# Kernel optimization log

Measured on AMD Instinct MI355X. Metric: run time of the kernel, lower is better.

Reference implementation:

```python
import jax, jax.numpy as jnp
import numpy as np

B, T, D, H = 8, 4096, 512, 512


def setup_inputs() -> dict:
    key = jax.random.key(0)
    k1, k2, k3, k4, k5, k6 = jax.random.split(key, 6)
    lim = 1.0 / np.sqrt(D)
    return {
        "x": jax.random.normal(k1, (B, T, D), dtype=jnp.float32),
        "h_0": jax.random.normal(k2, (B, 1, H), dtype=jnp.float32),
        "W_z": jax.random.uniform(k3, (H, D), jnp.float32, -lim, lim),
        "b_z": jax.random.uniform(k4, (H,), jnp.float32, -lim, lim),
        "W_h": jax.random.uniform(k5, (H, D), jnp.float32, -lim, lim),
        "b_h": jax.random.uniform(k6, (H,), jnp.float32, -lim, lim),
    }


def reference(x, h_0, W_z, b_z, W_h, b_h):
    # z_t = sigmoid(W_z x_t), h~_t = tanh(W_h x_t)
    z = jax.nn.sigmoid(jnp.einsum('btd,hd->bth', x, W_z) + b_z)  # (B,T,H)
    h_tilde = jnp.tanh(jnp.einsum('btd,hd->bth', x, W_h) + b_h)  # (B,T,H)
    a = 1.0 - z            # multiplicative coeffs
    b = z * h_tilde        # additive terms (b[:,0] handled as h0 carry)

    # linear recurrence h_t = a_t * h_{t-1} + b_t, h_0 given
    def scan_fn(h_prev, ab):
        a_t, b_t = ab
        h_t = a_t * h_prev + b_t
        return h_t, h_t

    a_t = jnp.swapaxes(a, 0, 1)  # (T,B,H)
    b_t = jnp.swapaxes(b, 0, 1)  # (T,B,H)
    _, hs = jax.lax.scan(scan_fn, h_0[:, 0, :], (a_t, b_t))
    return jnp.swapaxes(hs, 0, 1)  # (B,T,H)
```

## Files before the change

kernel.cpp:

```cpp
#include <hip/hip_runtime.h>

constexpr int Bn = 8, Tn = 4096, Dn = 512, Hn = 512;
constexpr int Mn = Bn * Tn;
constexpr int BM = 128, BHt = 128, BK = 32;
constexpr int NKT = Dn / BK;
constexpr int CH = 64, NC = Tn / CH;

typedef __attribute__((ext_vector_type(8))) short s8v;
typedef __attribute__((ext_vector_type(4))) float f4v;
typedef __attribute__((ext_vector_type(8))) _Float16 h8v;
typedef unsigned short ushort_t;

typedef __attribute__((address_space(1))) const void gv_t;
typedef __attribute__((address_space(3))) void lv_t;

__device__ __forceinline__ short f2bf(float f) {
  unsigned u = __float_as_uint(f);
  u = (u + 0x7fffu + ((u >> 16) & 1u)) >> 16;
  return (short)u;
}

__global__ __launch_bounds__(256) void convert_all(
    const float* __restrict__ X, const float* __restrict__ Wz,
    const float* __restrict__ Wh, ushort_t* __restrict__ Xb,
    ushort_t* __restrict__ Wzb, ushort_t* __restrict__ Whb) {
  int bx = blockIdx.x, tid = threadIdx.x;
  const float* src;
  ushort_t* dst;
  int lb;
  if (bx < 4096)      { src = X;  dst = Xb;  lb = bx; }
  else if (bx < 4160) { src = Wz; dst = Wzb; lb = bx - 4096; }
  else                { src = Wh; dst = Whb; lb = bx - 4160; }
  const float* tsrc = src + ((size_t)(lb >> 4) * 128) * Dn + (lb & 15) * BK;
#pragma unroll
  for (int p = 0; p < 2; p++) {
    int idx = tid + p * 256;
    int r = idx >> 2, k8 = idx & 3;
    const float4* sv = reinterpret_cast<const float4*>(tsrc + (size_t)r * Dn + k8 * 8);
    float4 f0 = sv[0], f1 = sv[1];
    s8v v;
    v[0] = f2bf(f0.x); v[1] = f2bf(f0.y); v[2] = f2bf(f0.z); v[3] = f2bf(f0.w);
    v[4] = f2bf(f1.x); v[5] = f2bf(f1.y); v[6] = f2bf(f1.z); v[7] = f2bf(f1.w);
    int c = (r >> 4) * 64 + k8 * 16 + (r & 15);
    *reinterpret_cast<s8v*>(&dst[((size_t)lb * 512 + c) * 8]) = v;
  }
}

__global__ __launch_bounds__(256) void gemm_act(
    const ushort_t* __restrict__ Xb, const ushort_t* __restrict__ Wzb,
    const ushort_t* __restrict__ Whb,
    const float* __restrict__ bzp, const float* __restrict__ bhp,
    h8v* __restrict__ cab) {
  __shared__ __align__(16) ushort_t lds[2][3 * 4096];

  int tid = threadIdx.x, lane = tid & 63, wid = tid >> 6;
  int wr = wid >> 1, wc = wid & 1;
  int bm = blockIdx.x, bhb = blockIdx.y;

  const ushort_t* xs = Xb + (size_t)bm * NKT * 4096;
  const ushort_t* zs = Wzb + (size_t)bhb * NKT * 4096;
  const ushort_t* hs = Whb + (size_t)bhb * NKT * 4096;

  f4v accz[4][4], acch[4][4];
#pragma unroll
  for (int i = 0; i < 4; i++)
#pragma unroll
    for (int j = 0; j < 4; j++) {
      accz[i][j] = (f4v){0.f, 0.f, 0.f, 0.f};
      acch[i][j] = (f4v){0.f, 0.f, 0.f, 0.f};
    }

  auto stage = [&](int buf, int ks) {
    ushort_t* l = lds[buf];
#pragma unroll
    for (int p = 0; p < 2; p++) {
      int off = p * 2048 + tid * 8;
      size_t go = (size_t)ks * 4096 + off;
      __builtin_amdgcn_global_load_lds((gv_t*)(xs + go), (lv_t*)(l + off), 16, 0, 0);
      __builtin_amdgcn_global_load_lds((gv_t*)(zs + go), (lv_t*)(l + 4096 + off), 16, 0, 0);
      __builtin_amdgcn_global_load_lds((gv_t*)(hs + go), (lv_t*)(l + 8192 + off), 16, 0, 0);
    }
  };

  stage(0, 0);
  for (int ks = 0; ks < NKT; ks++) {
    int cur = ks & 1;
    if (ks + 1 < NKT) {
      stage(cur ^ 1, ks + 1);
      asm volatile("s_waitcnt vmcnt(6)" ::: "memory");
    } else {
      asm volatile("s_waitcnt vmcnt(0)" ::: "memory");
    }
    __builtin_amdgcn_sched_barrier(0);
    __builtin_amdgcn_s_barrier();
    __builtin_amdgcn_sched_barrier(0);

    ushort_t* l = lds[cur];
    s8v af[4], bzf[4], bhf[4];
#pragma unroll
    for (int i = 0; i < 4; i++)
      af[i] = *reinterpret_cast<s8v*>(&l[((wr * 4 + i) * 64 + lane) * 8]);
#pragma unroll
    for (int j = 0; j < 4; j++) {
      bzf[j] = *reinterpret_cast<s8v*>(&l[4096 + ((wc * 4 + j) * 64 + lane) * 8]);
      bhf[j] = *reinterpret_cast<s8v*>(&l[8192 + ((wc * 4 + j) * 64 + lane) * 8]);
    }
#pragma unroll
    for (int i = 0; i < 4; i++)
#pragma unroll
      for (int j = 0; j < 4; j++) {
        accz[i][j] = __builtin_amdgcn_mfma_f32_16x16x32_bf16(af[i], bzf[j], accz[i][j], 0, 0, 0);
        acch[i][j] = __builtin_amdgcn_mfma_f32_16x16x32_bf16(af[i], bhf[j], acch[i][j], 0, 0, 0);
      }
    __builtin_amdgcn_sched_barrier(0);
    __builtin_amdgcn_s_barrier();
  }

  int R = bm * 2 + wr, Cc = bhb * 2 + wc;
  size_t base = (size_t)(R * 8 + Cc) * 1024;
  float bzv[4], bhv[4];
#pragma unroll
  for (int j = 0; j < 4; j++) {
    int h = bhb * BHt + wc * 64 + j * 16 + (lane & 15);
    bzv[j] = bzp[h];
    bhv[j] = bhp[h];
  }
#pragma unroll
  for (int i = 0; i < 4; i++)
#pragma unroll
    for (int j = 0; j < 4; j++) {
      h8v g;
#pragma unroll
      for (int q = 0; q < 4; q++) {
        float z = 1.f / (1.f + __expf(-(accz[i][j][q] + bzv[j])));
        float e = __expf(2.f * (acch[i][j][q] + bhv[j]));
        float th = 1.f - 2.f / (e + 1.f);
        g[q] = (_Float16)(1.f - z);
        g[4 + q] = (_Float16)(z * th);
      }
      cab[base + (size_t)((i * 4 + j) * 64 + lane)] = g;
    }
}

__global__ __launch_bounds__(256) void scan_chunk(
    const h8v* __restrict__ cab, float* __restrict__ cA, float* __restrict__ cB) {
  int h = blockIdx.y * 256 + threadIdx.x;
  int R = blockIdx.x;
  int hl = h & 63, Cc = h >> 6;
  size_t base = (size_t)(R * 8 + Cc) * 1024 + (size_t)(hl >> 4) * 64 + (hl & 15);
  float A = 1.f, Bv = 0.f;
#pragma unroll
  for (int i = 0; i < 4; i++)
#pragma unroll
    for (int p = 0; p < 4; p++) {
      h8v g = cab[base + i * 256 + p * 16];
#pragma unroll
      for (int q = 0; q < 4; q++) {
        float a = (float)g[q], b = (float)g[4 + q];
        A *= a;
        Bv = fmaf(a, Bv, b);
      }
    }
  cA[(size_t)R * Hn + h] = A;
  cB[(size_t)R * Hn + h] = Bv;
}

__global__ __launch_bounds__(256) void scan_heads(
    const float* __restrict__ cA, const float* __restrict__ cB,
    const float* __restrict__ h0p, float* __restrict__ hst) {
  int gid = blockIdx.x * 256 + threadIdx.x;
  int b = gid >> 9, h = gid & 511;
  float hr = h0p[(size_t)b * Hn + h];
#pragma unroll 8
  for (int c = 0; c < NC; c++) {
    size_t o = (size_t)(b * NC + c) * Hn + h;
    hst[o] = hr;
    hr = fmaf(cA[o], hr, cB[o]);
  }
}

__global__ __launch_bounds__(256) void scan_apply(
    const h8v* __restrict__ cab, const float* __restrict__ hst,
    float* __restrict__ out) {
  int h = blockIdx.y * 256 + threadIdx.x;
  int R = blockIdx.x;
  int hl = h & 63, Cc = h >> 6;
  size_t base = (size_t)(R * 8 + Cc) * 1024 + (size_t)(hl >> 4) * 64 + (hl & 15);
  float hr = hst[(size_t)R * Hn + h];
  size_t ob = (size_t)R * 64 * Hn + h;
#pragma unroll
  for (int i = 0; i < 4; i++)
#pragma unroll
    for (int p = 0; p < 4; p++) {
      h8v g = cab[base + i * 256 + p * 16];
#pragma unroll
      for (int q = 0; q < 4; q++) {
        hr = fmaf((float)g[q], hr, (float)g[4 + q]);
        out[ob + (size_t)(i * 16 + p * 4 + q) * Hn] = hr;
      }
    }
}

extern "C" void kernel_launch(void* const* d_in, const int* in_sizes, int n_in,
                              void* d_out, int out_size, void* d_ws, size_t ws_size,
                              hipStream_t stream) {
  const float* X   = (const float*)d_in[0];
  const float* h0p = (const float*)d_in[1];
  const float* Wz  = (const float*)d_in[2];
  const float* bz  = (const float*)d_in[3];
  const float* Wh  = (const float*)d_in[4];
  const float* bh  = (const float*)d_in[5];
  float* out = (float*)d_out;

  char* ws = (char*)d_ws;
  ushort_t* Xb  = (ushort_t*)ws;
  ushort_t* Wzb = Xb + (size_t)Mn * Dn;
  ushort_t* Whb = Wzb + (size_t)Hn * Dn;
  h8v* cab      = (h8v*)(Whb + (size_t)Hn * Dn);
  float* cA     = (float*)(cab + (size_t)Mn * Hn / 4);
  float* cB     = cA + (size_t)Bn * NC * Hn;
  float* hst    = cB + (size_t)Bn * NC * Hn;

  convert_all<<<dim3(4224), 256, 0, stream>>>(X, Wz, Wh, Xb, Wzb, Whb);

  gemm_act<<<dim3(Mn / BM, Hn / BHt), 256, 0, stream>>>(Xb, Wzb, Whb, bz, bh, cab);

  scan_chunk<<<dim3(Mn / 64, Hn / 256), 256, 0, stream>>>(cab, cA, cB);
  scan_heads<<<dim3(Bn * Hn / 256), 256, 0, stream>>>(cA, cB, h0p, hst);
  scan_apply<<<dim3(Mn / 64, Hn / 256), 256, 0, stream>>>(cab, hst, out);
}
```

Before: 111.3 us.

## Load GEMM fragments directly from global memory, dropping LDS staging and barriers

The gemm_act kernel no longer stages tiles of X, W_z and W_h through double-buffered LDS. Each wave now reads its MFMA fragments straight from the pre-swizzled global buffers, the loop is unrolled by two, and launch bounds request two blocks per CU. This removes the LDS traffic, waitcnt handling and block barriers, and may raise occupancy. In exchange, fragments that two waves share are read twice from global memory or cache, and there is no explicit prefetch to hide load latency.

```diff
diff --git a/kernel.cpp b/kernel.cpp
--- a/kernel.cpp
+++ b/kernel.cpp
@@ -10,9 +10,6 @@
 typedef __attribute__((ext_vector_type(4))) float f4v;
 typedef __attribute__((ext_vector_type(8))) _Float16 h8v;
 typedef unsigned short ushort_t;
-
-typedef __attribute__((address_space(1))) const void gv_t;
-typedef __attribute__((address_space(3))) void lv_t;
 
 __device__ __forceinline__ short f2bf(float f) {
   unsigned u = __float_as_uint(f);
@@ -46,20 +43,18 @@
   }
 }
 
-__global__ __launch_bounds__(256) void gemm_act(
+__global__ __launch_bounds__(256, 2) void gemm_act(
     const ushort_t* __restrict__ Xb, const ushort_t* __restrict__ Wzb,
     const ushort_t* __restrict__ Whb,
     const float* __restrict__ bzp, const float* __restrict__ bhp,
     h8v* __restrict__ cab) {
-  __shared__ __align__(16) ushort_t lds[2][3 * 4096];
-
   int tid = threadIdx.x, lane = tid & 63, wid = tid >> 6;
   int wr = wid >> 1, wc = wid & 1;
   int bm = blockIdx.x, bhb = blockIdx.y;
 
-  const ushort_t* xs = Xb + (size_t)bm * NKT * 4096;
-  const ushort_t* zs = Wzb + (size_t)bhb * NKT * 4096;
-  const ushort_t* hs = Whb + (size_t)bhb * NKT * 4096;
+  const s8v* xs = reinterpret_cast<const s8v*>(Xb) + (size_t)bm * NKT * 512 + (wr * 4) * 64 + lane;
+  const s8v* zs = reinterpret_cast<const s8v*>(Wzb) + (size_t)bhb * NKT * 512 + (wc * 4) * 64 + lane;
+  const s8v* hs = reinterpret_cast<const s8v*>(Whb) + (size_t)bhb * NKT * 512 + (wc * 4) * 64 + lane;
 
   f4v accz[4][4], acch[4][4];
 #pragma unroll
@@ -70,40 +65,15 @@
       acch[i][j] = (f4v){0.f, 0.f, 0.f, 0.f};
     }
 
-  auto stage = [&](int buf, int ks) {
-    ushort_t* l = lds[buf];
-#pragma unroll
-    for (int p = 0; p < 2; p++) {
-      int off = p * 2048 + tid * 8;
-      size_t go = (size_t)ks * 4096 + off;
-      __builtin_amdgcn_global_load_lds((gv_t*)(xs + go), (lv_t*)(l + off), 16, 0, 0);
-      __builtin_amdgcn_global_load_lds((gv_t*)(zs + go), (lv_t*)(l + 4096 + off), 16, 0, 0);
-      __builtin_amdgcn_global_load_lds((gv_t*)(hs + go), (lv_t*)(l + 8192 + off), 16, 0, 0);
-    }
-  };
-
-  stage(0, 0);
+#pragma unroll 2
   for (int ks = 0; ks < NKT; ks++) {
-    int cur = ks & 1;
-    if (ks + 1 < NKT) {
-      stage(cur ^ 1, ks + 1);
-      asm volatile("s_waitcnt vmcnt(6)" ::: "memory");
-    } else {
-      asm volatile("s_waitcnt vmcnt(0)" ::: "memory");
-    }
-    __builtin_amdgcn_sched_barrier(0);
-    __builtin_amdgcn_s_barrier();
-    __builtin_amdgcn_sched_barrier(0);
-
-    ushort_t* l = lds[cur];
     s8v af[4], bzf[4], bhf[4];
 #pragma unroll
-    for (int i = 0; i < 4; i++)
-      af[i] = *reinterpret_cast<s8v*>(&l[((wr * 4 + i) * 64 + lane) * 8]);
+    for (int i = 0; i < 4; i++) af[i] = xs[ks * 512 + i * 64];
 #pragma unroll
     for (int j = 0; j < 4; j++) {
-      bzf[j] = *reinterpret_cast<s8v*>(&l[4096 + ((wc * 4 + j) * 64 + lane) * 8]);
-      bhf[j] = *reinterpret_cast<s8v*>(&l[8192 + ((wc * 4 + j) * 64 + lane) * 8]);
+      bzf[j] = zs[ks * 512 + j * 64];
+      bhf[j] = hs[ks * 512 + j * 64];
     }
 #pragma unroll
     for (int i = 0; i < 4; i++)
@@ -112,8 +82,6 @@
         accz[i][j] = __builtin_amdgcn_mfma_f32_16x16x32_bf16(af[i], bzf[j], accz[i][j], 0, 0, 0);
         acch[i][j] = __builtin_amdgcn_mfma_f32_16x16x32_bf16(af[i], bhf[j], acch[i][j], 0, 0, 0);
       }
-    __builtin_amdgcn_sched_barrier(0);
-    __builtin_amdgcn_s_barrier();
   }
 
   int R = bm * 2 + wr, Cc = bhb * 2 + wc;
```

After: 105.7 us. -5.0%, faster.

## Fuse chunk-scan reduction into GEMM epilogue and enlarge GEMM tiles

Applied to the files above, without the earlier changes.

Removes the separate scan_chunk kernel by computing per-chunk (A,B) affine compositions inside the GEMM epilogue, using in-register products and cross-lane shuffles. The GEMM now uses 512-thread blocks with a 256-row tile and BK=64 per stage, an XCD-aware block remap, and setprio around the MFMAs. This avoids a full re-read of the cab intermediate and one launch, at the cost of more LDS (128KB), higher register pressure, and fewer blocks.

```diff
diff --git a/kernel.cpp b/kernel.cpp
--- a/kernel.cpp
+++ b/kernel.cpp
@@ -2,8 +2,7 @@
 
 constexpr int Bn = 8, Tn = 4096, Dn = 512, Hn = 512;
 constexpr int Mn = Bn * Tn;
-constexpr int BM = 128, BHt = 128, BK = 32;
-constexpr int NKT = Dn / BK;
+constexpr int NKT = Dn / 32;
 constexpr int CH = 64, NC = Tn / CH;
 
 typedef __attribute__((ext_vector_type(8))) short s8v;
@@ -31,7 +30,7 @@
   if (bx < 4096)      { src = X;  dst = Xb;  lb = bx; }
   else if (bx < 4160) { src = Wz; dst = Wzb; lb = bx - 4096; }
   else                { src = Wh; dst = Whb; lb = bx - 4160; }
-  const float* tsrc = src + ((size_t)(lb >> 4) * 128) * Dn + (lb & 15) * BK;
+  const float* tsrc = src + ((size_t)(lb >> 4) * 128) * Dn + (lb & 15) * 32;
 #pragma unroll
   for (int p = 0; p < 2; p++) {
     int idx = tid + p * 256;
@@ -46,20 +45,20 @@
   }
 }
 
-__global__ __launch_bounds__(256) void gemm_act(
+__global__ __launch_bounds__(512, 2) void gemm_act(
     const ushort_t* __restrict__ Xb, const ushort_t* __restrict__ Wzb,
     const ushort_t* __restrict__ Whb,
     const float* __restrict__ bzp, const float* __restrict__ bhp,
-    h8v* __restrict__ cab) {
-  __shared__ __align__(16) ushort_t lds[2][3 * 4096];
+    h8v* __restrict__ cab, float* __restrict__ cA, float* __restrict__ cB) {
+  __shared__ __align__(16) ushort_t lds[2 * 32768];
 
   int tid = threadIdx.x, lane = tid & 63, wid = tid >> 6;
   int wr = wid >> 1, wc = wid & 1;
-  int bm = blockIdx.x, bhb = blockIdx.y;
-
-  const ushort_t* xs = Xb + (size_t)bm * NKT * 4096;
-  const ushort_t* zs = Wzb + (size_t)bhb * NKT * 4096;
-  const ushort_t* hs = Whb + (size_t)bhb * NKT * 4096;
+
+  int o = blockIdx.x;
+  int wg = (o & 7) * 64 + (o >> 3);
+  int bm = wg & 127;
+  int bhb = wg >> 7;
 
   f4v accz[4][4], acch[4][4];
 #pragma unroll
@@ -71,23 +70,27 @@
     }
 
   auto stage = [&](int buf, int ks) {
-    ushort_t* l = lds[buf];
-#pragma unroll
-    for (int p = 0; p < 2; p++) {
-      int off = p * 2048 + tid * 8;
-      size_t go = (size_t)ks * 4096 + off;
-      __builtin_amdgcn_global_load_lds((gv_t*)(xs + go), (lv_t*)(l + off), 16, 0, 0);
-      __builtin_amdgcn_global_load_lds((gv_t*)(zs + go), (lv_t*)(l + 4096 + off), 16, 0, 0);
-      __builtin_amdgcn_global_load_lds((gv_t*)(hs + go), (lv_t*)(l + 8192 + off), 16, 0, 0);
+    ushort_t* l = lds + buf * 32768;
+#pragma unroll
+    for (int q = 0; q < 4; q++) {
+      const ushort_t* src = Xb + ((size_t)(bm * 2 + (q >> 1)) * 16 + (2 * ks + (q & 1))) * 4096 + tid * 8;
+      __builtin_amdgcn_global_load_lds((gv_t*)src, (lv_t*)(l + q * 4096 + tid * 8), 16, 0, 0);
+    }
+#pragma unroll
+    for (int q = 0; q < 2; q++) {
+      const ushort_t* sz = Wzb + ((size_t)bhb * 16 + 2 * ks + q) * 4096 + tid * 8;
+      __builtin_amdgcn_global_load_lds((gv_t*)sz, (lv_t*)(l + 16384 + q * 4096 + tid * 8), 16, 0, 0);
+      const ushort_t* sh = Whb + ((size_t)bhb * 16 + 2 * ks + q) * 4096 + tid * 8;
+      __builtin_amdgcn_global_load_lds((gv_t*)sh, (lv_t*)(l + 24576 + q * 4096 + tid * 8), 16, 0, 0);
     }
   };
 
   stage(0, 0);
-  for (int ks = 0; ks < NKT; ks++) {
+  for (int ks = 0; ks < 8; ks++) {
     int cur = ks & 1;
-    if (ks + 1 < NKT) {
+    if (ks < 7) {
       stage(cur ^ 1, ks + 1);
-      asm volatile("s_waitcnt vmcnt(6)" ::: "memory");
+      asm volatile("s_waitcnt vmcnt(8)" ::: "memory");
     } else {
       asm volatile("s_waitcnt vmcnt(0)" ::: "memory");
     }
@@ -95,41 +98,51 @@
     __builtin_amdgcn_s_barrier();
     __builtin_amdgcn_sched_barrier(0);
 
-    ushort_t* l = lds[cur];
-    s8v af[4], bzf[4], bhf[4];
-#pragma unroll
-    for (int i = 0; i < 4; i++)
-      af[i] = *reinterpret_cast<s8v*>(&l[((wr * 4 + i) * 64 + lane) * 8]);
-#pragma unroll
-    for (int j = 0; j < 4; j++) {
-      bzf[j] = *reinterpret_cast<s8v*>(&l[4096 + ((wc * 4 + j) * 64 + lane) * 8]);
-      bhf[j] = *reinterpret_cast<s8v*>(&l[8192 + ((wc * 4 + j) * 64 + lane) * 8]);
-    }
-#pragma unroll
-    for (int i = 0; i < 4; i++)
+    const ushort_t* l = lds + cur * 32768;
+#pragma unroll
+    for (int kk = 0; kk < 2; kk++) {
+      s8v af[4], bzf[4], bhf[4];
+#pragma unroll
+      for (int i = 0; i < 4; i++) {
+        int g = wr * 4 + i;
+        af[i] = *reinterpret_cast<const s8v*>(&l[(g >> 3) * 8192 + kk * 4096 + (g & 7) * 512 + lane * 8]);
+      }
 #pragma unroll
       for (int j = 0; j < 4; j++) {
-        accz[i][j] = __builtin_amdgcn_mfma_f32_16x16x32_bf16(af[i], bzf[j], accz[i][j], 0, 0, 0);
-        acch[i][j] = __builtin_amdgcn_mfma_f32_16x16x32_bf16(af[i], bhf[j], acch[i][j], 0, 0, 0);
-      }
+        int gj = wc * 4 + j;
+        bzf[j] = *reinterpret_cast<const s8v*>(&l[16384 + kk * 4096 + gj * 512 + lane * 8]);
+        bhf[j] = *reinterpret_cast<const s8v*>(&l[24576 + kk * 4096 + gj * 512 + lane * 8]);
+      }
+      __builtin_amdgcn_s_setprio(1);
+#pragma unroll
+      for (int i = 0; i < 4; i++)
+#pragma unroll
+        for (int j = 0; j < 4; j++) {
+          accz[i][j] = __builtin_amdgcn_mfma_f32_16x16x32_bf16(af[i], bzf[j], accz[i][j], 0, 0, 0);
+          acch[i][j] = __builtin_amdgcn_mfma_f32_16x16x32_bf16(af[i], bhf[j], acch[i][j], 0, 0, 0);
+        }
+      __builtin_amdgcn_s_setprio(0);
+    }
     __builtin_amdgcn_sched_barrier(0);
     __builtin_amdgcn_s_barrier();
   }
 
-  int R = bm * 2 + wr, Cc = bhb * 2 + wc;
+  int R = bm * 4 + wr, Cc = bhb * 2 + wc;
   size_t base = (size_t)(R * 8 + Cc) * 1024;
   float bzv[4], bhv[4];
 #pragma unroll
   for (int j = 0; j < 4; j++) {
-    int h = bhb * BHt + wc * 64 + j * 16 + (lane & 15);
+    int h = bhb * 128 + wc * 64 + j * 16 + (lane & 15);
     bzv[j] = bzp[h];
     bhv[j] = bhp[h];
   }
+  float QA[4][4], QB[4][4];
 #pragma unroll
   for (int i = 0; i < 4; i++)
 #pragma unroll
     for (int j = 0; j < 4; j++) {
       h8v g;
+      float Pa = 1.f, Pb = 0.f;
 #pragma unroll
       for (int q = 0; q < 4; q++) {
         float z = 1.f / (1.f + __expf(-(accz[i][j][q] + bzv[j])));
@@ -137,32 +150,40 @@
         float th = 1.f - 2.f / (e + 1.f);
         g[q] = (_Float16)(1.f - z);
         g[4 + q] = (_Float16)(z * th);
+        float a = (float)g[q], b = (float)g[4 + q];
+        Pa = a * Pa;
+        Pb = a * Pb + b;
       }
       cab[base + (size_t)((i * 4 + j) * 64 + lane)] = g;
-    }
-}
-
-__global__ __launch_bounds__(256) void scan_chunk(
-    const h8v* __restrict__ cab, float* __restrict__ cA, float* __restrict__ cB) {
-  int h = blockIdx.y * 256 + threadIdx.x;
-  int R = blockIdx.x;
-  int hl = h & 63, Cc = h >> 6;
-  size_t base = (size_t)(R * 8 + Cc) * 1024 + (size_t)(hl >> 4) * 64 + (hl & 15);
-  float A = 1.f, Bv = 0.f;
-#pragma unroll
-  for (int i = 0; i < 4; i++)
-#pragma unroll
-    for (int p = 0; p < 4; p++) {
-      h8v g = cab[base + i * 256 + p * 16];
-#pragma unroll
-      for (int q = 0; q < 4; q++) {
-        float a = (float)g[q], b = (float)g[4 + q];
-        A *= a;
-        Bv = fmaf(a, Bv, b);
-      }
-    }
-  cA[(size_t)R * Hn + h] = A;
-  cB[(size_t)R * Hn + h] = Bv;
+      QA[i][j] = Pa;
+      QB[i][j] = Pb;
+    }
+
+#pragma unroll
+  for (int j = 0; j < 4; j++) {
+    float A = 1.f, Bv = 0.f;
+#pragma unroll
+    for (int i = 0; i < 4; i++) {
+      float a = QA[i][j], b = QB[i][j];
+      float ap = __shfl_xor(a, 16), bp = __shfl_xor(b, 16);
+      bool hi = (lane & 16) != 0;
+      float af_ = hi ? ap : a, bf_ = hi ? bp : b;
+      float as_ = hi ? a : ap, bs_ = hi ? b : bp;
+      a = as_ * af_; b = as_ * bf_ + bs_;
+      ap = __shfl_xor(a, 32); bp = __shfl_xor(b, 32);
+      bool hi2 = (lane & 32) != 0;
+      af_ = hi2 ? ap : a; bf_ = hi2 ? bp : b;
+      as_ = hi2 ? a : ap; bs_ = hi2 ? b : bp;
+      a = as_ * af_; b = as_ * bf_ + bs_;
+      Bv = a * Bv + b;
+      A = a * A;
+    }
+    if (lane < 16) {
+      int h = bhb * 128 + wc * 64 + j * 16 + lane;
+      cA[(size_t)R * Hn + h] = A;
+      cB[(size_t)R * Hn + h] = Bv;
+    }
+  }
 }
 
 __global__ __launch_bounds__(256) void scan_heads(
@@ -223,9 +244,8 @@
 
   convert_all<<<dim3(4224), 256, 0, stream>>>(X, Wz, Wh, Xb, Wzb, Whb);
 
-  gemm_act<<<dim3(Mn / BM, Hn / BHt), 256, 0, stream>>>(Xb, Wzb, Whb, bz, bh, cab);
-
-  scan_chunk<<<dim3(Mn / 64, Hn / 256), 256, 0, stream>>>(cab, cA, cB);
+  gemm_act<<<dim3(512), 512, 0, stream>>>(Xb, Wzb, Whb, bz, bh, cab, cA, cB);
+
   scan_heads<<<dim3(Bn * Hn / 256), 256, 0, stream>>>(cA, cB, h0p, hst);
   scan_apply<<<dim3(Mn / 64, Hn / 256), 256, 0, stream>>>(cab, hst, out);
 }
```

Measured after the change: 102.0 us. 8.3% less time.
